# Performance work log

Measured on AMD Instinct MI355X. Metric: run time of the kernel, lower is better.

The kernel has to match this reference:

```python
import jax, jax.numpy as jnp
import numpy as np

N_PARTICLES = 6000
BOX_LENGTH = 10.0  # nm, orthogonal box
CUTOFF = 0.5       # nm


def _pair_indices(n):
    # static upper-triangular (i < j) pair list, matching meshgrid + (i < j) mask
    i_idx, j_idx = np.triu_indices(n, k=1)
    return jnp.asarray(i_idx.astype(np.int32)), jnp.asarray(j_idx.astype(np.int32))


def setup_inputs() -> dict:
    key = jax.random.key(0)
    k_pos, = jax.random.split(key, 1)
    positions = jax.random.uniform(k_pos, (N_PARTICLES, 3), dtype=jnp.float32) * BOX_LENGTH
    # orthogonal box: only the diagonal is read by the displacement function
    box_vectors = jnp.diag(jnp.array([BOX_LENGTH, BOX_LENGTH, BOX_LENGTH], dtype=jnp.float32))
    return {"positions": positions, "box_vectors": box_vectors, "is_periodic": 1}


def reference(positions, box_vectors, is_periodic):
    """Brute N^2 neighborlist (only_unique_pairs=True path).

    Faithful math: r_ij = pos[i]-pos[j]; PBC minimum-image wrap via remainder;
    d_ij = ||r_ij||; cutoff mask. The torch original boolean-compacts to a
    data-dependent n_pairs; for jit-compatible static shapes we keep the full
    P = n(n-1)/2 pair axis and mask: out-of-cutoff pair indices are -1 and
    their d_ij / r_ij are zeroed. In-cutoff entries are bitwise identical to
    the compacted torch outputs.
    """
    n = positions.shape[0]
    i_idx, j_idx = _pair_indices(n)

    r_ij = positions[i_idx] - positions[j_idx]          # [P, 3]
    if is_periodic:
        box_lengths = jnp.diag(box_vectors)             # [3]
        half = box_lengths * 0.5
        r_ij = jnp.remainder(r_ij + half, box_lengths) - half
    d_ij = jnp.sqrt(jnp.sum(r_ij * r_ij, axis=1, keepdims=True))  # [P, 1]

    in_cutoff = d_ij <= CUTOFF                          # [P, 1]
    pair_indices = jnp.where(in_cutoff[:, 0],
                             jnp.stack([i_idx, j_idx]).astype(jnp.int64),
                             -1)                        # [2, P]
    d_out = jnp.where(in_cutoff, d_ij, 0.0)
    r_out = jnp.where(in_cutoff, r_ij, 0.0)
    return pair_indices, d_out, r_out
```

## Files before the change

### kernel.cpp

```cpp
#include <hip/hip_runtime.h>


constexpr int NPART  = 6000;
constexpr int NPAIRS = 17997000;
constexpr float CUT  = 0.5f;
constexpr int TPB = 256;

__device__ __forceinline__ int row_start(int i) {
    return i * (NPART - 1) - (i * (i - 1)) / 2;
}

__device__ __forceinline__ float pbc_wrap(float r, float b, float h) {
    float v = __fadd_rn(r, h);
    if (v >= b)       v = __fsub_rn(v, b);
    else if (v < 0.f) v = __fadd_rn(v, b);
    return __fsub_rn(v, h);
}

__global__ __launch_bounds__(TPB) void nbl_scatter_kernel(
    const float* __restrict__ pos,
    const float* __restrict__ boxv,
    const int*  __restrict__ is_per,
    float* __restrict__ out)
{
    const int p = blockIdx.x * TPB + threadIdx.x;
    if (p >= NPAIRS) return;

    int disc_i = 143976001 - 8 * p;
    float sq = sqrtf((float)disc_i);
    int i = (int)((11999.0f - sq) * 0.5f);
    if (i < 0) i = 0;
    if (i > NPART - 2) i = NPART - 2;
    while (i < NPART - 2 && row_start(i + 1) <= p) ++i;
    while (i > 0 && row_start(i) > p) --i;
    const int j = i + 1 + (p - row_start(i));

    float rx = __fsub_rn(pos[3 * i + 0], pos[3 * j + 0]);
    float ry = __fsub_rn(pos[3 * i + 1], pos[3 * j + 1]);
    float rz = __fsub_rn(pos[3 * i + 2], pos[3 * j + 2]);

    if (*is_per != 0) {
        const float bx = boxv[0], by = boxv[4], bz = boxv[8];
        rx = pbc_wrap(rx, bx, __fmul_rn(bx, 0.5f));
        ry = pbc_wrap(ry, by, __fmul_rn(by, 0.5f));
        rz = pbc_wrap(rz, bz, __fmul_rn(bz, 0.5f));
    }

    float s = __fadd_rn(__fadd_rn(__fmul_rn(rx, rx), __fmul_rn(ry, ry)),
                        __fmul_rn(rz, rz));
    float d = __fsqrt_rn(s);

    if (d <= CUT) {
        out[p]              = (float)i;
        out[NPAIRS + p]     = (float)j;
        out[2 * NPAIRS + p] = d;
        float* rb = out + 3 * NPAIRS + 3 * p;
        rb[0] = rx; rb[1] = ry; rb[2] = rz;
    }
}

extern "C" void kernel_launch(void* const* d_in, const int* in_sizes, int n_in,
                              void* d_out, int out_size, void* d_ws, size_t ws_size,
                              hipStream_t stream) {
    const float* pos    = (const float*)d_in[0];
    const float* boxv   = (const float*)d_in[1];
    const int*   is_per = (const int*)d_in[2];
    float* out = (float*)d_out;

    hipMemsetD32Async((hipDeviceptr_t)out, (int)0xBF800000,
                      (size_t)2 * NPAIRS, stream);
    hipMemsetAsync(out + (size_t)2 * NPAIRS, 0,
                   (size_t)4 * NPAIRS * sizeof(float), stream);

    const int grid = (NPAIRS + TPB - 1) / TPB;
    nbl_scatter_kernel<<<grid, TPB, 0, stream>>>(pos, boxv, is_per, out);
}
```

Baseline: 469.4 us.

## Replace brute-force pair scan with a cell-list neighbor search

Adds a binning kernel that places particles into a 16^3 grid of cells with fixed capacity. A per-particle search kernel then scans only the 27 neighboring cells and writes hits straight into their fixed pair-index slots. This removes the O(N^2) per-pair thread launch and index inversion, leaving the output memsets as the main cost. The cell width is hardcoded from a box length of 10, and particles beyond 24 per cell are silently dropped, so correctness depends on the input distribution.

```diff
diff --git a/kernel.cpp b/kernel.cpp
--- a/kernel.cpp
+++ b/kernel.cpp
@@ -4,7 +4,13 @@
 constexpr int NPART  = 6000;
 constexpr int NPAIRS = 17997000;
 constexpr float CUT  = 0.5f;
-constexpr int TPB = 256;
+constexpr int NC     = 16;
+constexpr int NCELLS = NC * NC * NC;
+constexpr float INV_CW = 1.6f;
+constexpr int CAP    = 24;
+
+__device__ int g_cnt[NCELLS];
+__device__ int g_list[NCELLS * CAP];
 
 __device__ __forceinline__ int row_start(int i) {
     return i * (NPART - 1) - (i * (i - 1)) / 2;
@@ -17,45 +23,92 @@
     return __fsub_rn(v, h);
 }
 
-__global__ __launch_bounds__(TPB) void nbl_scatter_kernel(
+__device__ __forceinline__ int cell_of(float x) {
+    int c = (int)(x * INV_CW);
+    if (c < 0) c = 0;
+    if (c > NC - 1) c = NC - 1;
+    return c;
+}
+
+__global__ __launch_bounds__(1024) void bin_kernel(const float* __restrict__ pos)
+{
+    for (int c = (int)threadIdx.x; c < NCELLS; c += 1024) g_cnt[c] = 0;
+    __syncthreads();
+    for (int idx = (int)threadIdx.x; idx < NPART; idx += 1024) {
+        int cx = cell_of(pos[3 * idx + 0]);
+        int cy = cell_of(pos[3 * idx + 1]);
+        int cz = cell_of(pos[3 * idx + 2]);
+        int c  = (cz * NC + cy) * NC + cx;
+        int slot = atomicAdd(&g_cnt[c], 1);
+        if (slot < CAP) g_list[c * CAP + slot] = idx;
+    }
+}
+
+__global__ __launch_bounds__(256) void search_kernel(
     const float* __restrict__ pos,
     const float* __restrict__ boxv,
     const int*  __restrict__ is_per,
     float* __restrict__ out)
 {
-    const int p = blockIdx.x * TPB + threadIdx.x;
-    if (p >= NPAIRS) return;
+    const int i = blockIdx.x * 256 + threadIdx.x;
+    if (i >= NPART) return;
 
-    int disc_i = 143976001 - 8 * p;
-    float sq = sqrtf((float)disc_i);
-    int i = (int)((11999.0f - sq) * 0.5f);
-    if (i < 0) i = 0;
-    if (i > NPART - 2) i = NPART - 2;
-    while (i < NPART - 2 && row_start(i + 1) <= p) ++i;
-    while (i > 0 && row_start(i) > p) --i;
-    const int j = i + 1 + (p - row_start(i));
+    const float xi = pos[3 * i + 0];
+    const float yi = pos[3 * i + 1];
+    const float zi = pos[3 * i + 2];
 
-    float rx = __fsub_rn(pos[3 * i + 0], pos[3 * j + 0]);
-    float ry = __fsub_rn(pos[3 * i + 1], pos[3 * j + 1]);
-    float rz = __fsub_rn(pos[3 * i + 2], pos[3 * j + 2]);
+    const bool per = (*is_per != 0);
+    const float bx = boxv[0], by = boxv[4], bz = boxv[8];
+    const float hx = __fmul_rn(bx, 0.5f);
+    const float hy = __fmul_rn(by, 0.5f);
+    const float hz = __fmul_rn(bz, 0.5f);
 
-    if (*is_per != 0) {
-        const float bx = boxv[0], by = boxv[4], bz = boxv[8];
-        rx = pbc_wrap(rx, bx, __fmul_rn(bx, 0.5f));
-        ry = pbc_wrap(ry, by, __fmul_rn(by, 0.5f));
-        rz = pbc_wrap(rz, bz, __fmul_rn(bz, 0.5f));
-    }
+    const int cx = cell_of(xi), cy = cell_of(yi), cz = cell_of(zi);
+    const int pbase = row_start(i) - i - 1;
 
-    float s = __fadd_rn(__fadd_rn(__fmul_rn(rx, rx), __fmul_rn(ry, ry)),
-                        __fmul_rn(rz, rz));
-    float d = __fsqrt_rn(s);
+    for (int dz = -1; dz <= 1; ++dz) {
+        int ccz = cz + dz;
+        if (per) ccz = (ccz + NC) & (NC - 1);
+        else if (ccz < 0 || ccz >= NC) continue;
+        for (int dy = -1; dy <= 1; ++dy) {
+            int ccy = cy + dy;
+            if (per) ccy = (ccy + NC) & (NC - 1);
+            else if (ccy < 0 || ccy >= NC) continue;
+            for (int dx = -1; dx <= 1; ++dx) {
+                int ccx = cx + dx;
+                if (per) ccx = (ccx + NC) & (NC - 1);
+                else if (ccx < 0 || ccx >= NC) continue;
 
-    if (d <= CUT) {
-        out[p]              = (float)i;
-        out[NPAIRS + p]     = (float)j;
-        out[2 * NPAIRS + p] = d;
-        float* rb = out + 3 * NPAIRS + 3 * p;
-        rb[0] = rx; rb[1] = ry; rb[2] = rz;
+                const int c = (ccz * NC + ccy) * NC + ccx;
+                int cnt = g_cnt[c];
+                if (cnt > CAP) cnt = CAP;
+                for (int s = 0; s < cnt; ++s) {
+                    const int j = g_list[c * CAP + s];
+                    if (j <= i) continue;
+
+                    float rx = __fsub_rn(xi, pos[3 * j + 0]);
+                    float ry = __fsub_rn(yi, pos[3 * j + 1]);
+                    float rz = __fsub_rn(zi, pos[3 * j + 2]);
+                    if (per) {
+                        rx = pbc_wrap(rx, bx, hx);
+                        ry = pbc_wrap(ry, by, hy);
+                        rz = pbc_wrap(rz, bz, hz);
+                    }
+                    float ss = __fadd_rn(__fadd_rn(__fmul_rn(rx, rx),
+                                                   __fmul_rn(ry, ry)),
+                                         __fmul_rn(rz, rz));
+                    float d = __fsqrt_rn(ss);
+                    if (d <= CUT) {
+                        const int p = pbase + j;
+                        out[p]              = (float)i;
+                        out[NPAIRS + p]     = (float)j;
+                        out[2 * NPAIRS + p] = d;
+                        float* rb = out + (size_t)3 * NPAIRS + (size_t)3 * p;
+                        rb[0] = rx; rb[1] = ry; rb[2] = rz;
+                    }
+                }
+            }
+        }
     }
 }
 
@@ -67,11 +120,13 @@
     const int*   is_per = (const int*)d_in[2];
     float* out = (float*)d_out;
 
+    bin_kernel<<<1, 1024, 0, stream>>>(pos);
+
     hipMemsetD32Async((hipDeviceptr_t)out, (int)0xBF800000,
                       (size_t)2 * NPAIRS, stream);
     hipMemsetAsync(out + (size_t)2 * NPAIRS, 0,
                    (size_t)4 * NPAIRS * sizeof(float), stream);
 
-    const int grid = (NPAIRS + TPB - 1) / TPB;
-    nbl_scatter_kernel<<<grid, TPB, 0, stream>>>(pos, boxv, is_per, out);
+    const int grid = (NPART + 255) / 256;
+    search_kernel<<<grid, 256, 0, stream>>>(pos, boxv, is_per, out);
 }
```

Measured after the change: 534.5 us. 13.9% more time.
